# Optimization experiments

Measured on AMD Instinct MI355X. Metric: run time of the kernel, lower is better.

## Reference

```python
import jax, jax.numpy as jnp
import numpy as np

B, S, D, H = 4, 2048, 512, 8
DK = D // H


def setup_inputs() -> dict:
    key = jax.random.key(0)
    k1, k2, k3, k4 = jax.random.split(key, 4)
    return {
        "Zq": jax.random.normal(k1, (B, S, D), dtype=jnp.float32),
        "Zkv": jax.random.normal(k2, (B, S, D), dtype=jnp.float32),
        "mask": jnp.zeros((1, 1, S, S), dtype=jnp.float32),
        "Wqkv": jax.random.normal(k3, (D, 3 * D), dtype=jnp.float32),
        "Wout": jax.random.normal(k4, (D, D), dtype=jnp.float32),
    }


def reference(Zq, Zkv, mask, Wqkv, Wout):
    d_k = Wqkv.shape[0] // H
    Wq, Wk, Wv = jnp.split(Wqkv, 3, axis=-1)
    b, s, d = Zq.shape
    # project and split heads: [B,S,D] -> [B,H,S,dk]
    Q = (Zq @ Wq).reshape(b, s, H, d_k).transpose(0, 2, 1, 3)
    K = (Zkv @ Wk).reshape(b, s, H, d_k).transpose(0, 2, 1, 3)
    V = (Zkv @ Wv).reshape(b, s, H, d_k).transpose(0, 2, 1, 3)
    scale = d_k ** -0.5
    scores = jnp.einsum("bhqd,bhkd->bhqk", Q, K) * scale + mask
    attn = jax.nn.softmax(scores, axis=-1)  # [B,H,Sq,Skv]
    ctx = jnp.einsum("bhqk,bhkd->bhqd", attn, V)
    out = ctx.transpose(0, 2, 1, 3).reshape(b, s, d) @ Wout
    return out, attn.mean(axis=1)
```

## Files before the change

kernel.cpp:

```cpp
#include <hip/hip_runtime.h>
#include <cstdint>
#include <math.h>

#define B_ 4
#define S_ 2048
#define D_ 512
#define H_ 8
#define DK_ 64
#define SCALE 0.125f
#define INVLN2 1.4426950408889634f
#define QSCALE (SCALE * INVLN2)
#define KSTR 84
#define PSTR 68

using bfrag = __attribute__((ext_vector_type(8))) __bf16;
using b4    = __attribute__((ext_vector_type(4))) __bf16;
using f4    = __attribute__((ext_vector_type(4))) float;
using f2    = __attribute__((ext_vector_type(2))) float;
using f16v  = __attribute__((ext_vector_type(16))) float;
using u2    = __attribute__((ext_vector_type(2))) unsigned int;

#define MFMA16(a, b, c) __builtin_amdgcn_mfma_f32_16x16x32_bf16(a, b, c, 0, 0, 0)
#define MFMA32(a, b, c) __builtin_amdgcn_mfma_f32_32x32x16_bf16(a, b, c, 0, 0, 0)

__global__ __launch_bounds__(256) void wtr_all(
    const float* __restrict__ Wqkv, const float* __restrict__ Wout,
    __bf16* __restrict__ WqTh, __bf16* __restrict__ WqTl,
    __bf16* __restrict__ WkTh, __bf16* __restrict__ WkTl,
    __bf16* __restrict__ WvTh, __bf16* __restrict__ WoTh) {
  const int by = blockIdx.y;
  const int idx = blockIdx.x * 256 + threadIdx.x;
  const int k = idx & 511, n = idx >> 9;
  const float* W = (by == 3) ? Wout : Wqkv;
  const int ldw = (by == 3) ? 512 : 1536;
  const int c0 = (by == 3) ? 0 : by * 512;
  const float x = W[(size_t)k * ldw + c0 + n];
  const __bf16 h = (__bf16)x;
  __bf16* th = (by == 0) ? WqTh : (by == 1) ? WkTh : (by == 2) ? WvTh : WoTh;
  th[(size_t)n * 512 + k] = h;
  if (by < 2) {
    __bf16* tl = (by == 0) ? WqTl : WkTl;
    tl[(size_t)n * 512 + k] = (__bf16)(x - (float)h);
  }
}

__global__ __launch_bounds__(256) void qk_proj(
    const float* __restrict__ Zq, const float* __restrict__ Zkv,
    const __bf16* __restrict__ WqTh, const __bf16* __restrict__ WqTl,
    const __bf16* __restrict__ WkTh, const __bf16* __restrict__ WkTl,
    __bf16* __restrict__ Qh, __bf16* __restrict__ Ql,
    __bf16* __restrict__ Kh, __bf16* __restrict__ Kl) {
  __shared__ __bf16 Ash[64 * 40];
  __shared__ __bf16 Asl[64 * 40];
  __shared__ __bf16 Bsh[64 * 40];
  __shared__ __bf16 Bsl[64 * 40];

  const int zz = blockIdx.z;
  const float* A = zz ? Zkv : Zq;
  const __bf16* Bhp = zz ? WkTh : WqTh;
  const __bf16* Blp = zz ? WkTl : WqTl;
  __bf16* Oh = zz ? Kh : Qh;
  __bf16* Ol = zz ? Kl : Ql;
  const float cs = zz ? 1.0f : QSCALE;

  const int tid = threadIdx.x;
  const int m0 = blockIdx.y * 64, n0 = blockIdx.x * 64;
  const int row = tid >> 2, seg = tid & 3;
  const int lane = tid & 63, wv = tid >> 6;
  const int wm = (wv & 1) * 32, wn = (wv >> 1) * 32;
  const int qd = lane >> 4, ln = lane & 15;

  f4 acc[2][2];
#pragma unroll
  for (int i = 0; i < 2; i++)
#pragma unroll
    for (int j = 0; j < 2; j++)
#pragma unroll
      for (int r = 0; r < 4; r++) acc[i][j][r] = 0.f;

  for (int kt = 0; kt < 512; kt += 32) {
    const size_t abase = (size_t)(m0 + row) * 512 + kt + seg * 8;
    const size_t bbase = (size_t)(n0 + row) * 512 + kt + seg * 8;
    float4 a0 = *(const float4*)&A[abase];
    float4 a1 = *(const float4*)&A[abase + 4];
    float4 b0 = *(const float4*)&Bhp[bbase];
    float4 bl0 = *(const float4*)&Blp[bbase];
    __syncthreads();
    {
      float x[8] = {a0.x, a0.y, a0.z, a0.w, a1.x, a1.y, a1.z, a1.w};
      bfrag h, l;
#pragma unroll
      for (int j = 0; j < 8; j++) {
        h[j] = (__bf16)x[j];
        l[j] = (__bf16)(x[j] - (float)h[j]);
      }
      *(bfrag*)&Ash[row * 40 + seg * 8] = h;
      *(bfrag*)&Asl[row * 40 + seg * 8] = l;
    }
    *(float4*)&Bsh[row * 40 + seg * 8] = b0;
    *(float4*)&Bsl[row * 40 + seg * 8] = bl0;
    __syncthreads();

    bfrag ah[2], al[2], bh[2], bl[2];
#pragma unroll
    for (int mi = 0; mi < 2; mi++) {
      ah[mi] = *(bfrag*)&Ash[(wm + mi * 16 + ln) * 40 + qd * 8];
      al[mi] = *(bfrag*)&Asl[(wm + mi * 16 + ln) * 40 + qd * 8];
    }
#pragma unroll
    for (int ni = 0; ni < 2; ni++) {
      bh[ni] = *(bfrag*)&Bsh[(wn + ni * 16 + ln) * 40 + qd * 8];
      bl[ni] = *(bfrag*)&Bsl[(wn + ni * 16 + ln) * 40 + qd * 8];
    }
#pragma unroll
    for (int mi = 0; mi < 2; mi++)
#pragma unroll
      for (int ni = 0; ni < 2; ni++) {
        acc[mi][ni] = MFMA16(ah[mi], bh[ni], acc[mi][ni]);
        acc[mi][ni] = MFMA16(ah[mi], bl[ni], acc[mi][ni]);
        acc[mi][ni] = MFMA16(al[mi], bh[ni], acc[mi][ni]);
      }
  }

#pragma unroll
  for (int mi = 0; mi < 2; mi++)
#pragma unroll
    for (int ni = 0; ni < 2; ni++)
#pragma unroll
      for (int r = 0; r < 4; r++) {
        const int mrow = m0 + wm + mi * 16 + qd * 4 + r;
        const int ncol = n0 + wn + ni * 16 + ln;
        const float c = acc[mi][ni][r] * cs;
        const int b = mrow >> 11, s = mrow & (S_ - 1);
        const int h = ncol >> 6, dk = ncol & 63;
        const size_t o = (((size_t)b * H_ + h) * S_ + s) * DK_ + dk;
        __bf16 hh = (__bf16)c;
        Oh[o] = hh;
        Ol[o] = (__bf16)(c - (float)hh);
      }
}

template <bool AF32, bool BF32, bool LO, int MODE>
__global__ __launch_bounds__(256) void gemm_mfma(
    const void* __restrict__ Ap, const void* __restrict__ Bp, const void* __restrict__ Blop,
    float* __restrict__ Cf, __bf16* __restrict__ Oh, __bf16* __restrict__ Ol) {
  __shared__ __bf16 Ash[64 * 40];
  __shared__ __bf16 Asl[64 * 40];
  __shared__ __bf16 Bsh[64 * 40];
  __shared__ __bf16 Bsl[64 * 40];

  const int tid = threadIdx.x;
  const int m0 = blockIdx.y * 64, n0 = blockIdx.x * 64;
  const int row = tid >> 2, seg = tid & 3;
  const int lane = tid & 63, wv = tid >> 6;
  const int wm = (wv & 1) * 32, wn = (wv >> 1) * 32;
  const int qd = lane >> 4, ln = lane & 15;

  f4 acc[2][2];
#pragma unroll
  for (int i = 0; i < 2; i++)
#pragma unroll
    for (int j = 0; j < 2; j++)
#pragma unroll
      for (int r = 0; r < 4; r++) acc[i][j][r] = 0.f;

  for (int kt = 0; kt < 512; kt += 32) {
    const size_t abase = (size_t)(m0 + row) * 512 + kt + seg * 8;
    const size_t bbase = (size_t)(n0 + row) * 512 + kt + seg * 8;
    float4 a0, a1, b0, b1, bl0;
    if constexpr (AF32) {
      const float* A = (const float*)Ap;
      a0 = *(const float4*)&A[abase];
      a1 = *(const float4*)&A[abase + 4];
    } else {
      const __bf16* A = (const __bf16*)Ap;
      a0 = *(const float4*)&A[abase];
    }
    if constexpr (BF32) {
      const float* Bm = (const float*)Bp;
      b0 = *(const float4*)&Bm[bbase];
      b1 = *(const float4*)&Bm[bbase + 4];
    } else {
      const __bf16* Bm = (const __bf16*)Bp;
      b0 = *(const float4*)&Bm[bbase];
      if constexpr (LO) {
        const __bf16* Bl = (const __bf16*)Blop;
        bl0 = *(const float4*)&Bl[bbase];
      }
    }
    __syncthreads();
    if constexpr (AF32) {
      float x[8] = {a0.x, a0.y, a0.z, a0.w, a1.x, a1.y, a1.z, a1.w};
      bfrag h, l;
#pragma unroll
      for (int j = 0; j < 8; j++) {
        h[j] = (__bf16)x[j];
        l[j] = (__bf16)(x[j] - (float)h[j]);
      }
      *(bfrag*)&Ash[row * 40 + seg * 8] = h;
      if constexpr (LO) *(bfrag*)&Asl[row * 40 + seg * 8] = l;
    } else {
      *(float4*)&Ash[row * 40 + seg * 8] = a0;
    }
    if constexpr (BF32) {
      float x[8] = {b0.x, b0.y, b0.z, b0.w, b1.x, b1.y, b1.z, b1.w};
      bfrag h;
#pragma unroll
      for (int j = 0; j < 8; j++) h[j] = (__bf16)x[j];
      *(bfrag*)&Bsh[row * 40 + seg * 8] = h;
    } else {
      *(float4*)&Bsh[row * 40 + seg * 8] = b0;
      if constexpr (LO) *(float4*)&Bsl[row * 40 + seg * 8] = bl0;
    }
    __syncthreads();

    bfrag ah[2], al[2], bh[2], bl[2];
#pragma unroll
    for (int mi = 0; mi < 2; mi++) {
      ah[mi] = *(bfrag*)&Ash[(wm + mi * 16 + ln) * 40 + qd * 8];
      if constexpr (LO) al[mi] = *(bfrag*)&Asl[(wm + mi * 16 + ln) * 40 + qd * 8];
    }
#pragma unroll
    for (int ni = 0; ni < 2; ni++) {
      bh[ni] = *(bfrag*)&Bsh[(wn + ni * 16 + ln) * 40 + qd * 8];
      if constexpr (LO) bl[ni] = *(bfrag*)&Bsl[(wn + ni * 16 + ln) * 40 + qd * 8];
    }
#pragma unroll
    for (int mi = 0; mi < 2; mi++)
#pragma unroll
      for (int ni = 0; ni < 2; ni++) {
        acc[mi][ni] = MFMA16(ah[mi], bh[ni], acc[mi][ni]);
        if constexpr (LO) {
          acc[mi][ni] = MFMA16(ah[mi], bl[ni], acc[mi][ni]);
          acc[mi][ni] = MFMA16(al[mi], bh[ni], acc[mi][ni]);
        }
      }
  }

#pragma unroll
  for (int mi = 0; mi < 2; mi++)
#pragma unroll
    for (int ni = 0; ni < 2; ni++)
#pragma unroll
      for (int r = 0; r < 4; r++) {
        const int mrow = m0 + wm + mi * 16 + qd * 4 + r;
        const int ncol = n0 + wn + ni * 16 + ln;
        const float c = acc[mi][ni][r];
        if constexpr (MODE == 0) {
          Cf[(size_t)mrow * 512 + ncol] = c;
        } else if constexpr (MODE == 1) {
          const int b = mrow >> 11, s = mrow & (S_ - 1);
          const int h = ncol >> 6, dk = ncol & 63;
          const size_t o = (((size_t)b * H_ + h) * S_ + s) * DK_ + dk;
          __bf16 hh = (__bf16)c;
          Oh[o] = hh;
          Ol[o] = (__bf16)(c - (float)hh);
        } else {
          const int h = mrow >> 6, dk = mrow & 63;
          const int b = ncol >> 11, s = ncol & (S_ - 1);
          Oh[(((size_t)b * H_ + h) * DK_ + dk) * S_ + s] = (__bf16)c;
        }
      }
}

__global__ __launch_bounds__(256, 4) void attn_fctx(
    const __bf16* __restrict__ Qh_, const __bf16* __restrict__ Ql_,
    const __bf16* __restrict__ Kh_, const __bf16* __restrict__ Kl_,
    const __bf16* __restrict__ VT, const float* __restrict__ mask,
    __bf16* __restrict__ CTXb, float* __restrict__ MR, float* __restrict__ LR,
    unsigned char* __restrict__ E, float* __restrict__ MT) {
  __shared__ __bf16 Ksh[64 * KSTR];
  __shared__ __bf16 Ksl[64 * KSTR];
  __shared__ __bf16 Vs[64 * KSTR];
  __shared__ __bf16 Ps[128 * PSTR];
  __shared__ float als[128];
  const int tid = threadIdx.x, lane = tid & 63, wv = tid >> 6;
  const int l31 = lane & 31, kh = lane >> 5;
  const int qd = lane >> 4, ln = lane & 15;
  const int bh = blockIdx.y;
  const int q0b = blockIdx.x * 128;
  const int q0w = q0b + wv * 32;
  const int srow = tid >> 2, sseg = tid & 3;

  bfrag qhf[4], qlf[4];
#pragma unroll
  for (int ks = 0; ks < 4; ks++) {
    const size_t qb = ((size_t)bh * S_ + q0w + l31) * DK_ + ks * 16 + kh * 8;
    qhf[ks] = *(const bfrag*)&Qh_[qb];
    qlf[ks] = *(const bfrag*)&Ql_[qb];
  }

  float m = -3.0e38f, l = 0.f;
  f4 cacc[2][4];
#pragma unroll
  for (int mt = 0; mt < 2; mt++)
#pragma unroll
    for (int nt = 0; nt < 4; nt++)
#pragma unroll
      for (int r = 0; r < 4; r++) cacc[mt][nt][r] = 0.f;

  float4 h0, h1, l0, l1, v0, v1;
  {
    const size_t kb = ((size_t)bh * S_ + srow) * DK_ + sseg * 16;
    const size_t vb = ((size_t)bh * DK_ + srow) * S_ + sseg * 16;
    h0 = *(const float4*)&Kh_[kb]; h1 = *(const float4*)&Kh_[kb + 8];
    l0 = *(const float4*)&Kl_[kb]; l1 = *(const float4*)&Kl_[kb + 8];
    v0 = *(const float4*)&VT[vb];  v1 = *(const float4*)&VT[vb + 8];
  }

  for (int kt = 0; kt < S_; kt += 64) {
    __syncthreads();
    *(float4*)&Ksh[srow * KSTR + sseg * 16] = h0;
    *(float4*)&Ksh[srow * KSTR + sseg * 16 + 8] = h1;
    *(float4*)&Ksl[srow * KSTR + sseg * 16] = l0;
    *(float4*)&Ksl[srow * KSTR + sseg * 16 + 8] = l1;
    *(float4*)&Vs[srow * KSTR + sseg * 16] = v0;
    *(float4*)&Vs[srow * KSTR + sseg * 16 + 8] = v1;
    __syncthreads();

    f4 mk[2][4];
#pragma unroll
    for (int t = 0; t < 2; t++)
#pragma unroll
      for (int g = 0; g < 4; g++)
        mk[t][g] = *(const f4*)&mask[(size_t)(q0w + l31) * S_ + kt + t * 32 + g * 8 + 4 * kh];

    if (kt + 64 < S_) {
      const size_t kb = ((size_t)bh * S_ + kt + 64 + srow) * DK_ + sseg * 16;
      const size_t vb = ((size_t)bh * DK_ + srow) * S_ + kt + 64 + sseg * 16;
      h0 = *(const float4*)&Kh_[kb]; h1 = *(const float4*)&Kh_[kb + 8];
      l0 = *(const float4*)&Kl_[kb]; l1 = *(const float4*)&Kl_[kb + 8];
      v0 = *(const float4*)&VT[vb];  v1 = *(const float4*)&VT[vb + 8];
    }

    f16v z[2];
#pragma unroll
    for (int t = 0; t < 2; t++)
#pragma unroll
      for (int r = 0; r < 16; r++) z[t][r] = 0.f;
#pragma unroll
    for (int t = 0; t < 2; t++)
#pragma unroll
      for (int ks = 0; ks < 4; ks++) {
        bfrag kbh = *(bfrag*)&Ksh[(t * 32 + l31) * KSTR + ks * 16 + kh * 8];
        bfrag kbl = *(bfrag*)&Ksl[(t * 32 + l31) * KSTR + ks * 16 + kh * 8];
        z[t] = MFMA32(kbh, qhf[ks], z[t]);
        z[t] = MFMA32(kbl, qhf[ks], z[t]);
        z[t] = MFMA32(kbh, qlf[ks], z[t]);
      }

#pragma unroll
    for (int t = 0; t < 2; t++)
#pragma unroll
      for (int r = 0; r < 16; r++)
        z[t][r] = fmaf(mk[t][r >> 2][r & 3], INVLN2, z[t][r]);

    float tm = z[0][0];
#pragma unroll
    for (int t = 0; t < 2; t++)
#pragma unroll
      for (int r = 0; r < 16; r++) tm = fmaxf(tm, z[t][r]);
    tm = fmaxf(tm, __shfl_xor(tm, 32, 64));
    const bool need = (__any(tm > m) != 0);
    float al = 1.0f;
    if (need) {
      const float nm2 = fmaxf(m, tm);
      al = exp2f(m - nm2);
      m = nm2;
      if (lane < 32) als[wv * 32 + lane] = al;
    }
    const float nm = m;

    float ls = 0.f;
#pragma unroll
    for (int t = 0; t < 2; t++)
#pragma unroll
      for (int g = 0; g < 4; g++) {
        const float e0 = exp2f(z[t][g * 4 + 0] - nm);
        const float e1 = exp2f(z[t][g * 4 + 1] - nm);
        const float e2 = exp2f(z[t][g * 4 + 2] - nm);
        const float e3 = exp2f(z[t][g * 4 + 3] - nm);
        ls += (e0 + e1) + (e2 + e3);
        b4 pk;
        pk[0] = (__bf16)e0; pk[1] = (__bf16)e1;
        pk[2] = (__bf16)e2; pk[3] = (__bf16)e3;
        *(b4*)&Ps[(wv * 32 + l31) * PSTR + t * 32 + g * 8 + 4 * kh] = pk;
      }
    l = l * al + ls;

    if (lane < 32)
      MT[((size_t)bh * 32 + (kt >> 6)) * S_ + q0w + lane] = m;

    if (need) {
#pragma unroll
      for (int mt = 0; mt < 2; mt++) {
        f4 av = *(f4*)&als[wv * 32 + mt * 16 + qd * 4];
#pragma unroll
        for (int nt = 0; nt < 4; nt++)
#pragma unroll
          for (int r = 0; r < 4; r++) cacc[mt][nt][r] *= av[r];
      }
    }

    bfrag pa[2][2];
#pragma unroll
    for (int mt = 0; mt < 2; mt++)
#pragma unroll
      for (int ks = 0; ks < 2; ks++)
        pa[mt][ks] = *(bfrag*)&Ps[(wv * 32 + mt * 16 + ln) * PSTR + ks * 32 + qd * 8];
#pragma unroll
    for (int nt = 0; nt < 4; nt++)
#pragma unroll
      for (int ks = 0; ks < 2; ks++) {
        bfrag vbf = *(bfrag*)&Vs[(nt * 16 + ln) * KSTR + ks * 32 + qd * 8];
#pragma unroll
        for (int mt = 0; mt < 2; mt++)
          cacc[mt][nt] = MFMA16(pa[mt][ks], vbf, cacc[mt][nt]);
      }

#pragma unroll
    for (int c = 0; c < 4; c++) {
      const int row = wv * 32 + (lane >> 3) + c * 8;
      const int ch = lane & 7;
      bfrag pv = *(bfrag*)&Ps[row * PSTR + ch * 8];
      int lo = 0, hi = 0;
      lo = __builtin_amdgcn_cvt_pk_fp8_f32((float)pv[0], (float)pv[1], lo, 0);
      lo = __builtin_amdgcn_cvt_pk_fp8_f32((float)pv[2], (float)pv[3], lo, 1);
      hi = __builtin_amdgcn_cvt_pk_fp8_f32((float)pv[4], (float)pv[5], hi, 0);
      hi = __builtin_amdgcn_cvt_pk_fp8_f32((float)pv[6], (float)pv[7], hi, 1);
      u2 ev;
      ev.x = (unsigned int)lo;
      ev.y = (unsigned int)hi;
      __builtin_nontemporal_store(
          ev, (u2*)&E[((size_t)bh * S_ + q0b + row) * S_ + kt + ch * 8]);
    }
  }

  l += __shfl_xor(l, 32, 64);
  if (lane < 32) {
    MR[(size_t)bh * S_ + q0w + lane] = m;
    LR[(size_t)bh * S_ + q0w + lane] = l;
    als[wv * 32 + lane] = 1.0f / l;
  }
  const int b = bh >> 3, h = bh & 7;
#pragma unroll
  for (int mt = 0; mt < 2; mt++) {
    f4 iv = *(f4*)&als[wv * 32 + mt * 16 + qd * 4];
#pragma unroll
    for (int nt = 0; nt < 4; nt++)
#pragma unroll
      for (int r = 0; r < 4; r++)
        CTXb[((size_t)b * S_ + q0w + mt * 16 + qd * 4 + r) * D_ + h * DK_ + nt * 16 + ln] =
            (__bf16)(cacc[mt][nt][r] * iv[r]);
  }
}

__global__ __launch_bounds__(256) void mean_rescale(
    const unsigned char* __restrict__ E, const float* __restrict__ MT,
    const float* __restrict__ MR, const float* __restrict__ LR,
    float* __restrict__ meanout) {
  const int t = threadIdx.x;
  const int qr = t >> 3, seg = t & 7;
  const int b = blockIdx.y, ks = blockIdx.z;
  const int qg = blockIdx.x * 32 + qr;

  float mf[H_], il[H_];
#pragma unroll
  for (int h = 0; h < H_; h++) {
    const int bh = b * H_ + h;
    mf[h] = MR[(size_t)bh * S_ + qg];
    il[h] = 1.0f / LR[(size_t)bh * S_ + qg];
  }

  for (int kc = 0; kc < 8; kc++) {
    const int k0 = ks * 512 + kc * 64;
    const int tk = k0 >> 6;
    float acc[8];
#pragma unroll
    for (int j = 0; j < 8; j++) acc[j] = 0.f;
#pragma unroll
    for (int h = 0; h < H_; h++) {
      const int bh = b * H_ + h;
      const float mt = MT[((size_t)bh * 32 + tk) * S_ + qg];
      const float sc = exp2f(mt - mf[h]) * il[h];
      u2 e = __builtin_nontemporal_load(
          (const u2*)&E[((size_t)bh * S_ + qg) * S_ + k0 + seg * 8]);
      f2 p01 = __builtin_amdgcn_cvt_pk_f32_fp8((int)e.x, 0);
      f2 p23 = __builtin_amdgcn_cvt_pk_f32_fp8((int)e.x, 1);
      f2 p45 = __builtin_amdgcn_cvt_pk_f32_fp8((int)e.y, 0);
      f2 p67 = __builtin_amdgcn_cvt_pk_f32_fp8((int)e.y, 1);
      acc[0] += p01.x * sc; acc[1] += p01.y * sc;
      acc[2] += p23.x * sc; acc[3] += p23.y * sc;
      acc[4] += p45.x * sc; acc[5] += p45.y * sc;
      acc[6] += p67.x * sc; acc[7] += p67.y * sc;
    }
    f4 o0, o1;
    o0[0] = acc[0] * 0.125f; o0[1] = acc[1] * 0.125f;
    o0[2] = acc[2] * 0.125f; o0[3] = acc[3] * 0.125f;
    o1[0] = acc[4] * 0.125f; o1[1] = acc[5] * 0.125f;
    o1[2] = acc[6] * 0.125f; o1[3] = acc[7] * 0.125f;
    float* mp = &meanout[((size_t)b * S_ + qg) * S_ + k0 + seg * 8];
    *(f4*)&mp[0] = o0;
    *(f4*)&mp[4] = o1;
  }
}

extern "C" void kernel_launch(void* const* d_in, const int* in_sizes, int n_in,
                              void* d_out, int out_size, void* d_ws, size_t ws_size,
                              hipStream_t stream) {
  (void)in_sizes; (void)n_in; (void)out_size; (void)ws_size;
  const float* Zq = (const float*)d_in[0];
  const float* Zkv = (const float*)d_in[1];
  const float* mask = (const float*)d_in[2];
  const float* Wqkv = (const float*)d_in[3];
  const float* Wout = (const float*)d_in[4];

  float* out = (float*)d_out;
  float* mean = out + (size_t)B_ * S_ * D_;

  char* w = (char*)d_ws;
  const size_t WSZ = 512 * 512 * sizeof(__bf16);
  const size_t QSZ = (size_t)B_ * H_ * S_ * DK_ * sizeof(__bf16);
  __bf16* WqTh = (__bf16*)w; w += WSZ;
  __bf16* WqTl = (__bf16*)w; w += WSZ;
  __bf16* WkTh = (__bf16*)w; w += WSZ;
  __bf16* WkTl = (__bf16*)w; w += WSZ;
  __bf16* WvTh = (__bf16*)w; w += WSZ;
  __bf16* WoTh = (__bf16*)w; w += WSZ;
  __bf16* Qh = (__bf16*)w; w += QSZ;
  __bf16* Ql = (__bf16*)w; w += QSZ;
  __bf16* Kh = (__bf16*)w; w += QSZ;
  __bf16* Kl = (__bf16*)w; w += QSZ;
  __bf16* VTh = (__bf16*)w; w += QSZ;
  __bf16* CTXb = (__bf16*)w; w += QSZ;
  float* MR = (float*)w; w += (size_t)B_ * H_ * S_ * sizeof(float);
  float* LR = (float*)w; w += (size_t)B_ * H_ * S_ * sizeof(float);
  float* MT = (float*)w; w += (size_t)B_ * H_ * 32 * S_ * sizeof(float);
  unsigned char* E = (unsigned char*)w; w += (size_t)B_ * H_ * S_ * S_;

  wtr_all<<<dim3(1024, 4), 256, 0, stream>>>(Wqkv, Wout, WqTh, WqTl, WkTh, WkTl, WvTh, WoTh);

  qk_proj<<<dim3(8, 128, 2), 256, 0, stream>>>(
      Zq, Zkv, WqTh, WqTl, WkTh, WkTl, Qh, Ql, Kh, Kl);
  gemm_mfma<false, true, false, 2><<<dim3(128, 8), 256, 0, stream>>>(
      WvTh, Zkv, nullptr, nullptr, VTh, nullptr);

  attn_fctx<<<dim3(16, 32), 256, 0, stream>>>(Qh, Ql, Kh, Kl, VTh, mask, CTXb, MR, LR, E, MT);
  mean_rescale<<<dim3(64, 4, 4), 256, 0, stream>>>(E, MT, MR, LR, mean);

  gemm_mfma<false, false, false, 0><<<dim3(8, 128), 256, 0, stream>>>(
      CTXb, WoTh, nullptr, out, nullptr, nullptr);
}
```

Measured before the change: 456.1 us.

## Remodel mean_rescale thread mapping, drop conditional rescale, relax attention launch bounds

The mean_rescale kernel now gives each thread 16 contiguous keys of one query row. It loads them as one 16-byte FP8 chunk per head, making wider and more coalesced loads and stores, and launches four times as many blocks. In attn_fctx the wave-uniform branch that skipped the running-max rescale is removed, so the exp2 and the accumulator scaling always run. The launch-bounds occupancy hint of 4 is also dropped, which lets the compiler use more registers at the possible cost of occupancy.

```diff
diff --git a/kernel.cpp b/kernel.cpp
--- a/kernel.cpp
+++ b/kernel.cpp
@@ -19,6 +19,7 @@
 using f2    = __attribute__((ext_vector_type(2))) float;
 using f16v  = __attribute__((ext_vector_type(16))) float;
 using u2    = __attribute__((ext_vector_type(2))) unsigned int;
+using u4    = __attribute__((ext_vector_type(4))) unsigned int;
 
 #define MFMA16(a, b, c) __builtin_amdgcn_mfma_f32_16x16x32_bf16(a, b, c, 0, 0, 0)
 #define MFMA32(a, b, c) __builtin_amdgcn_mfma_f32_32x32x16_bf16(a, b, c, 0, 0, 0)
@@ -263,7 +264,7 @@
       }
 }
 
-__global__ __launch_bounds__(256, 4) void attn_fctx(
+__global__ __launch_bounds__(256) void attn_fctx(
     const __bf16* __restrict__ Qh_, const __bf16* __restrict__ Ql_,
     const __bf16* __restrict__ Kh_, const __bf16* __restrict__ Kl_,
     const __bf16* __restrict__ VT, const float* __restrict__ mask,
@@ -361,15 +362,10 @@
 #pragma unroll
       for (int r = 0; r < 16; r++) tm = fmaxf(tm, z[t][r]);
     tm = fmaxf(tm, __shfl_xor(tm, 32, 64));
-    const bool need = (__any(tm > m) != 0);
-    float al = 1.0f;
-    if (need) {
-      const float nm2 = fmaxf(m, tm);
-      al = exp2f(m - nm2);
-      m = nm2;
-      if (lane < 32) als[wv * 32 + lane] = al;
-    }
-    const float nm = m;
+    const float nm = fmaxf(m, tm);
+    const float al = exp2f(m - nm);
+    m = nm;
+    if (lane < 32) als[wv * 32 + lane] = al;
 
     float ls = 0.f;
 #pragma unroll
@@ -391,15 +387,13 @@
     if (lane < 32)
       MT[((size_t)bh * 32 + (kt >> 6)) * S_ + q0w + lane] = m;
 
-    if (need) {
-#pragma unroll
-      for (int mt = 0; mt < 2; mt++) {
-        f4 av = *(f4*)&als[wv * 32 + mt * 16 + qd * 4];
-#pragma unroll
-        for (int nt = 0; nt < 4; nt++)
-#pragma unroll
-          for (int r = 0; r < 4; r++) cacc[mt][nt][r] *= av[r];
-      }
+#pragma unroll
+    for (int mt = 0; mt < 2; mt++) {
+      f4 av = *(f4*)&als[wv * 32 + mt * 16 + qd * 4];
+#pragma unroll
+      for (int nt = 0; nt < 4; nt++)
+#pragma unroll
+        for (int r = 0; r < 4; r++) cacc[mt][nt][r] *= av[r];
     }
 
     bfrag pa[2][2];
@@ -460,48 +454,45 @@
     const float* __restrict__ MR, const float* __restrict__ LR,
     float* __restrict__ meanout) {
   const int t = threadIdx.x;
-  const int qr = t >> 3, seg = t & 7;
-  const int b = blockIdx.y, ks = blockIdx.z;
-  const int qg = blockIdx.x * 32 + qr;
-
-  float mf[H_], il[H_];
+  const int qr = t >> 5, sk = t & 31;
+  const int b = blockIdx.y;
+  const int qg = blockIdx.x * 8 + qr;
+  const int k0 = blockIdx.z * 512 + sk * 16;
+  const int tk = k0 >> 6;
+
+  float acc[16];
+#pragma unroll
+  for (int j = 0; j < 16; j++) acc[j] = 0.f;
+
 #pragma unroll
   for (int h = 0; h < H_; h++) {
     const int bh = b * H_ + h;
-    mf[h] = MR[(size_t)bh * S_ + qg];
-    il[h] = 1.0f / LR[(size_t)bh * S_ + qg];
-  }
-
-  for (int kc = 0; kc < 8; kc++) {
-    const int k0 = ks * 512 + kc * 64;
-    const int tk = k0 >> 6;
-    float acc[8];
-#pragma unroll
-    for (int j = 0; j < 8; j++) acc[j] = 0.f;
-#pragma unroll
-    for (int h = 0; h < H_; h++) {
-      const int bh = b * H_ + h;
-      const float mt = MT[((size_t)bh * 32 + tk) * S_ + qg];
-      const float sc = exp2f(mt - mf[h]) * il[h];
-      u2 e = __builtin_nontemporal_load(
-          (const u2*)&E[((size_t)bh * S_ + qg) * S_ + k0 + seg * 8]);
-      f2 p01 = __builtin_amdgcn_cvt_pk_f32_fp8((int)e.x, 0);
-      f2 p23 = __builtin_amdgcn_cvt_pk_f32_fp8((int)e.x, 1);
-      f2 p45 = __builtin_amdgcn_cvt_pk_f32_fp8((int)e.y, 0);
-      f2 p67 = __builtin_amdgcn_cvt_pk_f32_fp8((int)e.y, 1);
-      acc[0] += p01.x * sc; acc[1] += p01.y * sc;
-      acc[2] += p23.x * sc; acc[3] += p23.y * sc;
-      acc[4] += p45.x * sc; acc[5] += p45.y * sc;
-      acc[6] += p67.x * sc; acc[7] += p67.y * sc;
-    }
-    f4 o0, o1;
-    o0[0] = acc[0] * 0.125f; o0[1] = acc[1] * 0.125f;
-    o0[2] = acc[2] * 0.125f; o0[3] = acc[3] * 0.125f;
-    o1[0] = acc[4] * 0.125f; o1[1] = acc[5] * 0.125f;
-    o1[2] = acc[6] * 0.125f; o1[3] = acc[7] * 0.125f;
-    float* mp = &meanout[((size_t)b * S_ + qg) * S_ + k0 + seg * 8];
-    *(f4*)&mp[0] = o0;
-    *(f4*)&mp[4] = o1;
+    const float mf = MR[(size_t)bh * S_ + qg];
+    const float il = 1.0f / LR[(size_t)bh * S_ + qg];
+    const float mt = MT[((size_t)bh * 32 + tk) * S_ + qg];
+    const float sc = exp2f(mt - mf) * il;
+    u4 e = __builtin_nontemporal_load(
+        (const u4*)&E[((size_t)bh * S_ + qg) * S_ + k0]);
+#pragma unroll
+    for (int wd = 0; wd < 4; wd++) {
+      f2 plo = __builtin_amdgcn_cvt_pk_f32_fp8((int)e[wd], 0);
+      f2 phi = __builtin_amdgcn_cvt_pk_f32_fp8((int)e[wd], 1);
+      acc[wd * 4 + 0] += plo.x * sc;
+      acc[wd * 4 + 1] += plo.y * sc;
+      acc[wd * 4 + 2] += phi.x * sc;
+      acc[wd * 4 + 3] += phi.y * sc;
+    }
+  }
+
+  float* mp = &meanout[((size_t)b * S_ + qg) * S_ + k0];
+#pragma unroll
+  for (int wd = 0; wd < 4; wd++) {
+    f4 o;
+    o[0] = acc[wd * 4 + 0] * 0.125f;
+    o[1] = acc[wd * 4 + 1] * 0.125f;
+    o[2] = acc[wd * 4 + 2] * 0.125f;
+    o[3] = acc[wd * 4 + 3] * 0.125f;
+    *(f4*)&mp[wd * 4] = o;
   }
 }
 
@@ -546,7 +537,7 @@
       WvTh, Zkv, nullptr, nullptr, VTh, nullptr);
 
   attn_fctx<<<dim3(16, 32), 256, 0, stream>>>(Qh, Ql, Kh, Kl, VTh, mask, CTXb, MR, LR, E, MT);
-  mean_rescale<<<dim3(64, 4, 4), 256, 0, stream>>>(E, MT, MR, LR, mean);
+  mean_rescale<<<dim3(256, 4, 4), 256, 0, stream>>>(E, MT, MR, LR, mean);
 
   gemm_mfma<false, false, false, 0><<<dim3(8, 128), 256, 0, stream>>>(
       CTXb, WoTh, nullptr, out, nullptr, nullptr);
```

Result: faster. 383.8 us (-15.9%).
